# Kernel optimization log

Hardware: AMD Instinct MI355X
Metric: run time of the kernel (lower is better)

The kernel has to match this reference:

```python
import jax, jax.numpy as jnp
from jax import lax
import numpy as np

DECAY = 0.9               # sft_teacher_memory_decay default
ATTN_TEMP = 0.07          # attention_temperature default
COS_EPS = 1e-6            # torch cosine_similarity eps

B, F, T, D = 2, 32, 1024, 1024
H = W = 512


def setup_inputs() -> dict:
    key = jax.random.key(0)
    k1, k2 = jax.random.split(key)
    frame_tokens = jax.random.normal(k1, (B, F, T, D), dtype=jnp.float32)
    frame_masks = jax.random.uniform(k2, (B, F, H, W), dtype=jnp.float32)
    return {"frame_tokens": frame_tokens, "frame_masks": frame_masks}


def _tracker_memory(frame_tokens, frame_masks):
    # mask coverage per frame: [B, F, 1, 1]
    cov = jnp.mean(jnp.clip(frame_masks, 0.0, 1.0), axis=(-1, -2))[..., None, None]
    base_blend = 1.0 - DECAY

    toks = jnp.swapaxes(frame_tokens, 0, 1)  # [F, B, T, D]
    covs = jnp.swapaxes(cov, 0, 1)           # [F, B, 1, 1]
    init = toks[0]                            # [B, T, D]

    def step(memory, xs):
        current, coverage = xs  # [B,T,D], [B,1,1]
        # torch cosine_similarity(dim=-1, eps): dot / (max(|a|,eps)*max(|b|,eps))
        num = jnp.sum(current * memory, axis=-1)                       # [B,T]
        n_cur = jnp.maximum(jnp.sqrt(jnp.sum(current * current, axis=-1)), COS_EPS)
        n_mem = jnp.maximum(jnp.sqrt(jnp.sum(memory * memory, axis=-1)), COS_EPS)
        sim = (num / (n_cur * n_mem))[..., None]                       # [B,T,1]
        gate = jax.nn.sigmoid(sim / ATTN_TEMP)
        gate = gate * (0.5 + 0.5 * coverage)                           # mask-aware frame gate
        blend = jnp.clip(base_blend * (0.5 + gate), 0.0, 1.0)
        memory = memory + blend * (current - memory)
        return memory, memory

    _, outs = lax.scan(step, init, (toks[1:], covs[1:]))
    result = jnp.concatenate([init[None], outs], axis=0)  # [F, B, T, D]
    return jnp.swapaxes(result, 0, 1)                      # [B, F, T, D]


def reference(frame_tokens, frame_masks):
    return _tracker_memory(frame_tokens, frame_masks)
```

## Files before the change

kernel.cpp:

```cpp
#include <hip/hip_runtime.h>
#include <math.h>

namespace {
constexpr int B = 2, F = 32, T = 1024, D = 1024;
constexpr int H = 512, W = 512;
constexpr int HWN = H * W;
constexpr float BASE_BLEND = 0.1f;
constexpr float COS_EPS = 1e-6f;
constexpr int COV_SUB = 16;
}

__global__ __launch_bounds__(256) void cov_partial_kernel(
    const float* __restrict__ masks, float* __restrict__ partial) {
  const int s   = blockIdx.x >> 4;
  const int sub = blockIdx.x & (COV_SUB - 1);
  const float4* p = reinterpret_cast<const float4*>(masks) +
                    (size_t)s * (HWN / 4) + (size_t)sub * (HWN / 4 / COV_SUB);
  float sum = 0.f;
#pragma unroll
  for (int i = 0; i < 16; ++i) {
    float4 v = p[i * 256 + threadIdx.x];
    sum += fminf(fmaxf(v.x, 0.f), 1.f);
    sum += fminf(fmaxf(v.y, 0.f), 1.f);
    sum += fminf(fmaxf(v.z, 0.f), 1.f);
    sum += fminf(fmaxf(v.w, 0.f), 1.f);
  }
#pragma unroll
  for (int m = 32; m; m >>= 1) sum += __shfl_xor(sum, m, 64);
  __shared__ float sw[4];
  if ((threadIdx.x & 63) == 0) sw[threadIdx.x >> 6] = sum;
  __syncthreads();
  if (threadIdx.x == 0) partial[blockIdx.x] = sw[0] + sw[1] + sw[2] + sw[3];
}

__global__ void cov_final_kernel(const float* __restrict__ partial,
                                 float* __restrict__ cov) {
  const int i = threadIdx.x;
  float s = 0.f;
#pragma unroll
  for (int j = 0; j < COV_SUB; ++j) s += partial[i * COV_SUB + j];
  cov[i] = s * (1.0f / (float)HWN);
}

#define DOT4(a, b) ((a).x * (b).x + (a).y * (b).y + (a).z * (b).z + (a).w * (b).w)
#define EMA4(m, c, bl)                 \
  do {                                 \
    (m).x += (bl) * ((c).x - (m).x);   \
    (m).y += (bl) * ((c).y - (m).y);   \
    (m).z += (bl) * ((c).z - (m).z);   \
    (m).w += (bl) * ((c).w - (m).w);   \
  } while (0)

__global__ __launch_bounds__(256) void tracker_kernel(
    const float4* __restrict__ toks, const float* __restrict__ cov,
    float4* __restrict__ out) {
  const int tid  = threadIdx.x;
  const int wv   = tid >> 6;
  const int lane = tid & 63;
  const int r    = blockIdx.x * 4 + wv;
  const int b    = r >> 10;
  const int t    = r & 1023;

  const size_t rowbase = ((size_t)b * F * T + (size_t)t) * (D / 4);
  const size_t fs      = (size_t)T * (D / 4);
  const float4* tp = toks + rowbase + lane;
  float4*       op = out  + rowbase + lane;
  const float* covp = cov + b * F;

  float4 m0 = tp[0],  m1 = tp[64], m2 = tp[128], m3 = tp[192];
  op[0] = m0; op[64] = m1; op[128] = m2; op[192] = m3;

  float4 c0 = tp[fs], c1 = tp[fs + 64], c2 = tp[fs + 128], c3 = tp[fs + 192];

  for (int f = 1; f < F; ++f) {
    float4 n0, n1, n2, n3;
    if (f + 1 < F) {
      const float4* np = tp + (size_t)(f + 1) * fs;
      n0 = np[0]; n1 = np[64]; n2 = np[128]; n3 = np[192];
    }

    float dot = DOT4(c0, m0) + DOT4(c1, m1) + DOT4(c2, m2) + DOT4(c3, m3);
    float nc  = DOT4(c0, c0) + DOT4(c1, c1) + DOT4(c2, c2) + DOT4(c3, c3);
    float nm  = DOT4(m0, m0) + DOT4(m1, m1) + DOT4(m2, m2) + DOT4(m3, m3);

#pragma unroll
    for (int msk = 32; msk; msk >>= 1) {
      dot += __shfl_xor(dot, msk, 64);
      nc  += __shfl_xor(nc,  msk, 64);
      nm  += __shfl_xor(nm,  msk, 64);
    }

    const float sim = dot / (fmaxf(sqrtf(nc), COS_EPS) * fmaxf(sqrtf(nm), COS_EPS));
    float gate = 1.0f / (1.0f + expf(-sim / 0.07f));
    gate *= 0.5f + 0.5f * covp[f];
    float bl = BASE_BLEND * (0.5f + gate);
    bl = fminf(fmaxf(bl, 0.0f), 1.0f);

    EMA4(m0, c0, bl); EMA4(m1, c1, bl); EMA4(m2, c2, bl); EMA4(m3, c3, bl);

    float4* o = op + (size_t)f * fs;
    o[0] = m0; o[64] = m1; o[128] = m2; o[192] = m3;

    c0 = n0; c1 = n1; c2 = n2; c3 = n3;
  }
}

extern "C" void kernel_launch(void* const* d_in, const int* in_sizes, int n_in,
                              void* d_out, int out_size, void* d_ws, size_t ws_size,
                              hipStream_t stream) {
  const float* toks  = (const float*)d_in[0];
  const float* masks = (const float*)d_in[1];
  float* out = (float*)d_out;

  float* partial = (float*)d_ws;
  float* cov     = partial + B * F * COV_SUB;

  cov_partial_kernel<<<B * F * COV_SUB, 256, 0, stream>>>(masks, partial);
  cov_final_kernel<<<1, 64, 0, stream>>>(partial, cov);
  tracker_kernel<<<(B * T) / 4, 256, 0, stream>>>(
      (const float4*)toks, cov, (float4*)out);
}
```

Before: 473.7 us.

## Assign one block per token row with cross-wave shared-memory reduction

Each token row is now processed by a full 256-thread block holding one float4 per thread, instead of one 64-lane wave holding four float4s per lane. The grid grows fourfold to 2048 blocks, which raises the number of independent rows in flight for this memory-bound scan. In exchange, every frame step needs a shared-memory cross-wave reduction and a __syncthreads, and each thread has fewer outstanding loads. A double-buffered slot array avoids a second barrier per step.

```diff
diff --git a/kernel.cpp b/kernel.cpp
--- a/kernel.cpp
+++ b/kernel.cpp
@@ -43,52 +43,51 @@
 }
 
 #define DOT4(a, b) ((a).x * (b).x + (a).y * (b).y + (a).z * (b).z + (a).w * (b).w)
-#define EMA4(m, c, bl)                 \
-  do {                                 \
-    (m).x += (bl) * ((c).x - (m).x);   \
-    (m).y += (bl) * ((c).y - (m).y);   \
-    (m).z += (bl) * ((c).z - (m).z);   \
-    (m).w += (bl) * ((c).w - (m).w);   \
-  } while (0)
 
 __global__ __launch_bounds__(256) void tracker_kernel(
     const float4* __restrict__ toks, const float* __restrict__ cov,
     float4* __restrict__ out) {
-  const int tid  = threadIdx.x;
-  const int wv   = tid >> 6;
-  const int lane = tid & 63;
-  const int r    = blockIdx.x * 4 + wv;
-  const int b    = r >> 10;
-  const int t    = r & 1023;
+  const int tid = threadIdx.x;
+  const int wv  = tid >> 6;
+  const int r   = blockIdx.x;
+  const int b   = r >> 10;
 
-  const size_t rowbase = ((size_t)b * F * T + (size_t)t) * (D / 4);
+  const size_t rowbase = ((size_t)(b * F * T) + (size_t)(r & 1023)) * (D / 4);
   const size_t fs      = (size_t)T * (D / 4);
-  const float4* tp = toks + rowbase + lane;
-  float4*       op = out  + rowbase + lane;
+  const float4* tp = toks + rowbase + tid;
+  float4*       op = out  + rowbase + tid;
   const float* covp = cov + b * F;
 
-  float4 m0 = tp[0],  m1 = tp[64], m2 = tp[128], m3 = tp[192];
-  op[0] = m0; op[64] = m1; op[128] = m2; op[192] = m3;
+  __shared__ float red[2][4][3];
 
-  float4 c0 = tp[fs], c1 = tp[fs + 64], c2 = tp[fs + 128], c3 = tp[fs + 192];
+  float4 m = tp[0];
+  op[0] = m;
+
+  float4 c = tp[fs];
 
   for (int f = 1; f < F; ++f) {
-    float4 n0, n1, n2, n3;
-    if (f + 1 < F) {
-      const float4* np = tp + (size_t)(f + 1) * fs;
-      n0 = np[0]; n1 = np[64]; n2 = np[128]; n3 = np[192];
-    }
+    float4 n;
+    if (f + 1 < F) n = tp[(size_t)(f + 1) * fs];
 
-    float dot = DOT4(c0, m0) + DOT4(c1, m1) + DOT4(c2, m2) + DOT4(c3, m3);
-    float nc  = DOT4(c0, c0) + DOT4(c1, c1) + DOT4(c2, c2) + DOT4(c3, c3);
-    float nm  = DOT4(m0, m0) + DOT4(m1, m1) + DOT4(m2, m2) + DOT4(m3, m3);
-
+    float dot = DOT4(c, m);
+    float nc  = DOT4(c, c);
+    float nm  = DOT4(m, m);
 #pragma unroll
     for (int msk = 32; msk; msk >>= 1) {
       dot += __shfl_xor(dot, msk, 64);
       nc  += __shfl_xor(nc,  msk, 64);
       nm  += __shfl_xor(nm,  msk, 64);
     }
+    const int slot = f & 1;
+    if ((tid & 63) == 0) {
+      red[slot][wv][0] = dot;
+      red[slot][wv][1] = nc;
+      red[slot][wv][2] = nm;
+    }
+    __syncthreads();
+    dot = red[slot][0][0] + red[slot][1][0] + red[slot][2][0] + red[slot][3][0];
+    nc  = red[slot][0][1] + red[slot][1][1] + red[slot][2][1] + red[slot][3][1];
+    nm  = red[slot][0][2] + red[slot][1][2] + red[slot][2][2] + red[slot][3][2];
 
     const float sim = dot / (fmaxf(sqrtf(nc), COS_EPS) * fmaxf(sqrtf(nm), COS_EPS));
     float gate = 1.0f / (1.0f + expf(-sim / 0.07f));
@@ -96,12 +95,13 @@
     float bl = BASE_BLEND * (0.5f + gate);
     bl = fminf(fmaxf(bl, 0.0f), 1.0f);
 
-    EMA4(m0, c0, bl); EMA4(m1, c1, bl); EMA4(m2, c2, bl); EMA4(m3, c3, bl);
+    m.x += bl * (c.x - m.x);
+    m.y += bl * (c.y - m.y);
+    m.z += bl * (c.z - m.z);
+    m.w += bl * (c.w - m.w);
 
-    float4* o = op + (size_t)f * fs;
-    o[0] = m0; o[64] = m1; o[128] = m2; o[192] = m3;
-
-    c0 = n0; c1 = n1; c2 = n2; c3 = n3;
+    op[(size_t)f * fs] = m;
+    c = n;
   }
 }
 
@@ -117,6 +117,6 @@
 
   cov_partial_kernel<<<B * F * COV_SUB, 256, 0, stream>>>(masks, partial);
   cov_final_kernel<<<1, 64, 0, stream>>>(partial, cov);
-  tracker_kernel<<<(B * T) / 4, 256, 0, stream>>>(
+  tracker_kernel<<<B * T, 256, 0, stream>>>(
       (const float4*)toks, cov, (float4*)out);
 }
```

New measurement: 477.7 us. No clear change (+0.9%).
